# Optimization experiments

Hardware: AMD Instinct MI355X
Metric: run time of the kernel (lower is better)

## Reference

```python
import jax, jax.numpy as jnp
import numpy as np

DIM = 2048
N_HEADS = 32
N_KV_HEADS = 8
HEAD_DIM = DIM // N_HEADS  # 64
MAX_SEQ_LEN = 2048
ROPE_THETA = 10000.0
ROPE_SCALE = 1.0  # ("linear", 1.0)


def build_rope_cache(seq_len):
    # standard half-rotation RoPE cache with linear position scaling
    inv_freq = 1.0 / (ROPE_THETA ** (jnp.arange(0, HEAD_DIM, 2, dtype=jnp.float32) / HEAD_DIM))
    t = jnp.arange(seq_len, dtype=jnp.float32) / ROPE_SCALE
    freqs = jnp.outer(t, inv_freq)                      # [S, HD/2]
    emb = jnp.concatenate([freqs, freqs], axis=-1)      # [S, HD]
    return jnp.cos(emb), jnp.sin(emb)


def apply_rope(x, cos, sin):
    # x: [B, S, H, D]; cos/sin: [S, D]
    c = cos[None, :, None, :]
    s = sin[None, :, None, :]
    x1, x2 = jnp.split(x, 2, axis=-1)
    rot = jnp.concatenate([-x2, x1], axis=-1)           # rotate_half
    return x * c + rot * s


def setup_inputs() -> dict:
    key = jax.random.key(0)
    kx, kq, kk, kv, ko = jax.random.split(key, 5)
    B, S = 1, 2048
    x = jax.random.normal(kx, (B, S, DIM), dtype=jnp.float32)
    # nn.Linear weights stored [out_features, in_features]
    wq = jax.random.normal(kq, (DIM, DIM), dtype=jnp.float32) * 0.02
    wk = jax.random.normal(kk, (HEAD_DIM * N_KV_HEADS, DIM), dtype=jnp.float32) * 0.02
    wv = jax.random.normal(kv, (HEAD_DIM * N_KV_HEADS, DIM), dtype=jnp.float32) * 0.02
    wo = jax.random.normal(ko, (DIM, DIM), dtype=jnp.float32) * 0.02
    return {"x": x, "wq": wq, "wk": wk, "wv": wv, "wo": wo}


def reference(x, wq, wk, wv, wo):
    B, S, _ = x.shape
    g = N_HEADS // N_KV_HEADS  # GQA expand factor
    q = (x @ wq.T).reshape(B, S, N_HEADS, HEAD_DIM)
    k = (x @ wk.T).reshape(B, S, N_KV_HEADS, HEAD_DIM)
    v = (x @ wv.T).reshape(B, S, N_KV_HEADS, HEAD_DIM)
    cos, sin = build_rope_cache(S)
    q = apply_rope(q, cos, sin)
    k = apply_rope(k, cos, sin)
    # group q heads with their kv head instead of repeat_interleave on k/v
    q = q.transpose(0, 2, 1, 3).reshape(B, N_KV_HEADS, g, S, HEAD_DIM)
    k = k.transpose(0, 2, 1, 3)   # [B, Hkv, S, D]
    v = v.transpose(0, 2, 1, 3)
    scale = 1.0 / jnp.sqrt(jnp.asarray(HEAD_DIM, dtype=x.dtype))
    scores = jnp.einsum('bhgqd,bhkd->bhgqk', q, k) * scale  # [B,Hkv,g,S,S]
    causal = jnp.tril(jnp.ones((S, S), dtype=bool))
    scores = jnp.where(causal[None, None, None, :, :], scores, -jnp.inf)
    p = jax.nn.softmax(scores, axis=-1)
    out = jnp.einsum('bhgqk,bhkd->bhgqd', p, v)             # [B,Hkv,g,S,D]
    out = out.reshape(B, N_HEADS, S, HEAD_DIM).transpose(0, 2, 1, 3).reshape(B, S, DIM)
    return out @ wo.T
```

## Files before the change

kernel.cpp:

```cpp
#include <hip/hip_runtime.h>
#include <hip/hip_bf16.h>
#include <cstdint>
#include <cstddef>

#define DIM_ 2048
#define SLEN 2048
#define NQH 32
#define NKVH 8
#define HDIM 64
#define KVDIM 512

typedef __attribute__((ext_vector_type(8))) short short8;
typedef __attribute__((ext_vector_type(4))) float f32x4;
typedef __attribute__((ext_vector_type(16))) float f32x16;
typedef __attribute__((ext_vector_type(4))) unsigned int u32x4;

#define QSCALE 0.1803368801111243f

__device__ __forceinline__ unsigned short f2bf(float f) {
  unsigned u = __builtin_bit_cast(unsigned, f);
  u += 0x7FFFu + ((u >> 16) & 1u);
  return (unsigned short)(u >> 16);
}

__device__ __forceinline__ unsigned pack2bf(float a, float b) {
  return ((unsigned)f2bf(b) << 16) | (unsigned)f2bf(a);
}

__device__ __forceinline__ void gload_lds16(const void* g, void* l) {
  __builtin_amdgcn_global_load_lds(
      (const __attribute__((address_space(1))) void*)g,
      (__attribute__((address_space(3))) void*)l, 16, 0, 0);
}

__global__ void cvt_bf16_kernel(const float* __restrict__ in,
                                unsigned short* __restrict__ out, int n) {
  int i = (blockIdx.x * blockDim.x + threadIdx.x) * 8;
  if (i >= n) return;
  float4 a = *(const float4*)(in + i);
  float4 b = *(const float4*)(in + i + 4);
  ushort4 o0, o1;
  o0.x = f2bf(a.x); o0.y = f2bf(a.y); o0.z = f2bf(a.z); o0.w = f2bf(a.w);
  o1.x = f2bf(b.x); o1.y = f2bf(b.y); o1.z = f2bf(b.z); o1.w = f2bf(b.w);
  *(ushort4*)(out + i) = o0;
  *(ushort4*)(out + i + 4) = o1;
}

__global__ void rope_table_kernel(float* __restrict__ cosT, float* __restrict__ sinT) {
  int idx = blockIdx.x * blockDim.x + threadIdx.x;
  int s = idx >> 5, i = idx & 31;
  float inv = expf(-(float)i * (9.210340371976184f / 32.0f));
  float fr = (float)s * inv;
  cosT[idx] = cosf(fr);
  sinT[idx] = sinf(fr);
}

__global__ __launch_bounds__(256, 2)
void gemm_qkv(const unsigned short* __restrict__ A,
              const unsigned short* __restrict__ B,
              unsigned short* __restrict__ Qr,
              unsigned short* __restrict__ Kr,
              unsigned short* __restrict__ Vtp,
              const float* __restrict__ cosT,
              const float* __restrict__ sinT) {
  constexpr int K = DIM_;
  __shared__ unsigned short sA[128 * 32];
  __shared__ unsigned short sB[128 * 32];
  const int tid = threadIdx.x;
  const int wv = tid >> 6, ln = tid & 63;
  const int row0 = blockIdx.x * 128;
  const int col0 = blockIdx.y * 128;
  const int wr = (wv >> 1) * 64, wc = (wv & 1) * 64;
  const int lrow = ln & 15, lk = (ln >> 4) * 8;
  f32x4 acc[4][4] = {};

  for (int kt = 0; kt < K; kt += 32) {
#pragma unroll
    for (int r = 0; r < 2; ++r) {
      int e = (r * 256 + tid) * 8;
      int rr = e >> 5, cc = e & 31;
      gload_lds16(A + (size_t)(row0 + rr) * K + kt + cc,
                  sA + (size_t)(r * 256 + wv * 64) * 8);
      gload_lds16(B + (size_t)(col0 + rr) * K + kt + cc,
                  sB + (size_t)(r * 256 + wv * 64) * 8);
    }
    __syncthreads();
    short8 af[4], bfr[4];
#pragma unroll
    for (int m = 0; m < 4; ++m)
      af[m] = *(const short8*)(sA + (wr + m * 16 + lrow) * 32 + lk);
#pragma unroll
    for (int n = 0; n < 4; ++n)
      bfr[n] = *(const short8*)(sB + (wc + n * 16 + lrow) * 32 + lk);
#pragma unroll
    for (int m = 0; m < 4; ++m)
#pragma unroll
      for (int n = 0; n < 4; ++n)
        acc[m][n] = __builtin_amdgcn_mfma_f32_16x16x32_bf16(af[m], bfr[n],
                                                            acc[m][n], 0, 0, 0);
    __syncthreads();
  }
  const int orow = (ln >> 4) * 4;
  const int by = blockIdx.y;
  if (by < 16) {
#pragma unroll
    for (int m = 0; m < 4; ++m)
#pragma unroll
      for (int j = 0; j < 4; ++j) {
        const int s = row0 + wr + m * 16 + orow + j;
#pragma unroll
        for (int n = 0; n < 2; ++n) {
          const int d1 = n * 16 + lrow;
          const float cv = cosT[s * 32 + d1], sv = sinT[s * 32 + d1];
          const float x1 = acc[m][n][j], x2 = acc[m][n + 2][j];
          const size_t base = (size_t)s * DIM_ + col0 + wc + d1;
          Qr[base] = f2bf((x1 * cv - x2 * sv) * QSCALE);
          Qr[base + 32] = f2bf((x2 * cv + x1 * sv) * QSCALE);
        }
      }
  } else if (by < 20) {
    const int cb = col0 - 2048;
#pragma unroll
    for (int m = 0; m < 4; ++m)
#pragma unroll
      for (int j = 0; j < 4; ++j) {
        const int s = row0 + wr + m * 16 + orow + j;
#pragma unroll
        for (int n = 0; n < 2; ++n) {
          const int d1 = n * 16 + lrow;
          const float cv = cosT[s * 32 + d1], sv = sinT[s * 32 + d1];
          const float x1 = acc[m][n][j], x2 = acc[m][n + 2][j];
          const size_t base = (size_t)s * KVDIM + cb + wc + d1;
          Kr[base] = f2bf(x1 * cv - x2 * sv);
          Kr[base + 32] = f2bf(x2 * cv + x1 * sv);
        }
      }
  } else {
    const int cb = col0 - 2560;
#pragma unroll
    for (int m = 0; m < 4; ++m)
#pragma unroll
      for (int n = 0; n < 4; ++n)
#pragma unroll
        for (int j = 0; j < 4; ++j) {
          const int s = row0 + wr + m * 16 + orow + j;
          const int vc = cb + wc + n * 16 + lrow;
          Vtp[(size_t)vc * SLEN + s] = f2bf(acc[m][n][j]);
        }
  }
}

__global__ __launch_bounds__(256, 2)
void gemm_bt_f32(const unsigned short* __restrict__ A,
                 const unsigned short* __restrict__ B, float* __restrict__ C) {
  constexpr int K = DIM_;
  __shared__ unsigned short sA[128 * 32];
  __shared__ unsigned short sB[128 * 32];
  const int tid = threadIdx.x;
  const int wv = tid >> 6, ln = tid & 63;
  const int row0 = blockIdx.x * 128;
  const int col0 = blockIdx.y * 128;
  const int wr = (wv >> 1) * 64, wc = (wv & 1) * 64;
  const int lrow = ln & 15, lk = (ln >> 4) * 8;
  f32x4 acc[4][4] = {};
  for (int kt = 0; kt < K; kt += 32) {
#pragma unroll
    for (int r = 0; r < 2; ++r) {
      int e = (r * 256 + tid) * 8;
      int rr = e >> 5, cc = e & 31;
      gload_lds16(A + (size_t)(row0 + rr) * K + kt + cc,
                  sA + (size_t)(r * 256 + wv * 64) * 8);
      gload_lds16(B + (size_t)(col0 + rr) * K + kt + cc,
                  sB + (size_t)(r * 256 + wv * 64) * 8);
    }
    __syncthreads();
    short8 af[4], bfr[4];
#pragma unroll
    for (int m = 0; m < 4; ++m)
      af[m] = *(const short8*)(sA + (wr + m * 16 + lrow) * 32 + lk);
#pragma unroll
    for (int n = 0; n < 4; ++n)
      bfr[n] = *(const short8*)(sB + (wc + n * 16 + lrow) * 32 + lk);
#pragma unroll
    for (int m = 0; m < 4; ++m)
#pragma unroll
      for (int n = 0; n < 4; ++n)
        acc[m][n] = __builtin_amdgcn_mfma_f32_16x16x32_bf16(af[m], bfr[n],
                                                            acc[m][n], 0, 0, 0);
    __syncthreads();
  }
  const int orow = (ln >> 4) * 4;
#pragma unroll
  for (int m = 0; m < 4; ++m)
#pragma unroll
    for (int n = 0; n < 4; ++n)
#pragma unroll
      for (int j = 0; j < 4; ++j)
        C[(size_t)(row0 + wr + m * 16 + orow + j) * DIM_ + col0 + wc + n * 16 + lrow] =
            acc[m][n][j];
}

__global__ __launch_bounds__(256, 2)
void attn2_kernel(const unsigned short* __restrict__ Q,
                  const unsigned short* __restrict__ Kc,
                  const unsigned short* __restrict__ Vt,
                  unsigned short* __restrict__ AO) {
  __shared__ __align__(16) char smem[32768];
  const int b = blockIdx.x, h = blockIdx.y;
  const int kvh = h >> 2;
  const int tid = threadIdx.x;
  const int w = tid >> 6, l = tid & 63;
  const int l31 = l & 31, hi = l >> 5;
  const int kvcol = kvh * HDIM;

  int srow[2], scolb[2];
#pragma unroll
  for (int r = 0; r < 2; ++r) {
    int L = (r * 256 + tid) * 16;
    int row = L >> 7;
    srow[r] = row;
    scolb[r] = (L & 127) ^ ((row & 7) << 4);
  }

  for (int pass = 0; pass < 2; ++pass) {
    const int c = pass ? (15 - b) : b;
    const int nt = (c + 1) * 2;
    const int wq0 = c * 128 + w * 32;
    const int qrow = wq0 + l31;

    short8 qf[4];
    {
      const unsigned short* qp = Q + (size_t)qrow * DIM_ + h * HDIM + hi * 8;
#pragma unroll
      for (int dblk = 0; dblk < 4; ++dblk) qf[dblk] = *(const short8*)(qp + dblk * 16);
    }
    f32x16 o[2] = {};
    float mrun = -1e30f, lrun = 0.f;

#pragma unroll
    for (int r = 0; r < 2; ++r) {
      gload_lds16((const char*)Kc + (((size_t)srow[r] * KVDIM + kvcol) << 1) + scolb[r],
                  smem + r * 4096 + w * 1024);
      gload_lds16((const char*)Vt + (((size_t)(kvcol + srow[r]) * SLEN) << 1) + scolb[r],
                  smem + 16384 + r * 4096 + w * 1024);
    }
    __syncthreads();

    for (int t = 0; t < nt; ++t) {
      const int cur = t & 1;
      const int k0 = t * 64;
      if (t + 1 < nt) {
        const int nb = cur ^ 1;
        const int k0n = k0 + 64;
#pragma unroll
        for (int r = 0; r < 2; ++r) {
          gload_lds16((const char*)Kc + (((size_t)(k0n + srow[r]) * KVDIM + kvcol) << 1) + scolb[r],
                      smem + nb * 8192 + r * 4096 + w * 1024);
          gload_lds16((const char*)Vt + (((size_t)(kvcol + srow[r]) * SLEN + k0n) << 1) + scolb[r],
                      smem + 16384 + nb * 8192 + r * 4096 + w * 1024);
        }
      }
      if (k0 <= wq0 + 31) {
        const char* sK = smem + cur * 8192;
        const char* sV = smem + 16384 + cur * 8192;
        f32x16 s0 = {}, s1 = {};
        __builtin_amdgcn_s_setprio(1);
#pragma unroll
        for (int dblk = 0; dblk < 4; ++dblk) {
          const int colb = (dblk * 32 + hi * 16) ^ ((l31 & 7) << 4);
          short8 kf0 = *(const short8*)(sK + l31 * 128 + colb);
          short8 kf1 = *(const short8*)(sK + (32 + l31) * 128 + colb);
          s0 = __builtin_amdgcn_mfma_f32_32x32x16_bf16(kf0, qf[dblk], s0, 0, 0, 0);
          s1 = __builtin_amdgcn_mfma_f32_32x32x16_bf16(kf1, qf[dblk], s1, 0, 0, 0);
        }
        __builtin_amdgcn_s_setprio(0);

        float p[32];
#pragma unroll
        for (int r = 0; r < 16; ++r) { p[r] = s0[r]; p[16 + r] = s1[r]; }
        if (k0 + 63 > wq0) {
#pragma unroll
          for (int r = 0; r < 16; ++r) {
            const int ka = k0 + (r & 3) + 8 * (r >> 2) + 4 * hi;
            if (ka > qrow) p[r] = -1e30f;
            if (ka + 32 > qrow) p[16 + r] = -1e30f;
          }
        }
        float mt = p[0];
#pragma unroll
        for (int i = 1; i < 32; ++i) mt = fmaxf(mt, p[i]);
        mt = fmaxf(mt, __shfl_xor(mt, 32));
        const float mnew = fmaxf(mrun, mt);
        const float alpha = exp2f(mrun - mnew);
        mrun = mnew;
        float rs = 0.f;
#pragma unroll
        for (int i = 0; i < 32; ++i) { p[i] = exp2f(p[i] - mnew); rs += p[i]; }
        rs += __shfl_xor(rs, 32);
        lrun = lrun * alpha + rs;
#pragma unroll
        for (int r = 0; r < 16; ++r) { o[0][r] *= alpha; o[1][r] *= alpha; }

        unsigned pa[8], pb[8], sa[8], sb[8];
#pragma unroll
        for (int i = 0; i < 8; ++i) {
          pa[i] = pack2bf(p[i * 4 + 0], p[i * 4 + 1]);
          pb[i] = pack2bf(p[i * 4 + 2], p[i * 4 + 3]);
        }
#pragma unroll
        for (int i = 0; i < 8; ++i) {
          sa[i] = __shfl_xor((int)pa[i], 32);
          sb[i] = __shfl_xor((int)pb[i], 32);
        }
        __builtin_amdgcn_s_setprio(1);
#pragma unroll
        for (int kb = 0; kb < 4; ++kb) {
          const int i0 = (kb >> 1) * 4 + (kb & 1) * 2;
          const int i1 = i0 + 1;
          const unsigned w0 = hi ? sa[i1] : pa[i0];
          const unsigned w1 = hi ? sb[i1] : pb[i0];
          const unsigned w2 = hi ? pa[i1] : sa[i0];
          const unsigned w3 = hi ? pb[i1] : sb[i0];
          u32x4 uu = {w0, w1, w2, w3};
          short8 pf = __builtin_bit_cast(short8, uu);
          const int colb = (kb * 32 + hi * 16) ^ ((l31 & 7) << 4);
          short8 vf0 = *(const short8*)(sV + l31 * 128 + colb);
          short8 vf1 = *(const short8*)(sV + (32 + l31) * 128 + colb);
          o[0] = __builtin_amdgcn_mfma_f32_32x32x16_bf16(vf0, pf, o[0], 0, 0, 0);
          o[1] = __builtin_amdgcn_mfma_f32_32x32x16_bf16(vf1, pf, o[1], 0, 0, 0);
        }
        __builtin_amdgcn_s_setprio(0);
      }
      __syncthreads();
    }

    const float inv = 1.0f / lrun;
    char* tw = smem + w * 4096;
#pragma unroll
    for (int db = 0; db < 2; ++db)
#pragma unroll
      for (int g = 0; g < 4; ++g) {
        ushort4 v;
        v.x = f2bf(o[db][g * 4 + 0] * inv);
        v.y = f2bf(o[db][g * 4 + 1] * inv);
        v.z = f2bf(o[db][g * 4 + 2] * inv);
        v.w = f2bf(o[db][g * 4 + 3] * inv);
        const int d0 = db * 32 + g * 8 + hi * 4;
        *(ushort4*)(tw + l31 * 128 + ((d0 * 2) ^ ((l31 & 7) << 4))) = v;
      }
    {
      const int rr = l >> 1, cc = (l & 1) * 32;
      unsigned short* ap = AO + (size_t)(c * 128 + w * 32 + rr) * DIM_ + h * HDIM + cc;
#pragma unroll
      for (int pq = 0; pq < 4; ++pq) {
        const int colb = ((cc + pq * 8) * 2) ^ ((rr & 7) << 4);
        short8 v = *(const short8*)(tw + rr * 128 + colb);
        *(short8*)(ap + pq * 8) = v;
      }
    }
    __syncthreads();
  }
}

extern "C" void kernel_launch(void* const* d_in, const int* in_sizes, int n_in,
                              void* d_out, int out_size, void* d_ws, size_t ws_size,
                              hipStream_t stream) {
  const float* x  = (const float*)d_in[0];
  const float* wq = (const float*)d_in[1];
  const float* wk = (const float*)d_in[2];
  const float* wv = (const float*)d_in[3];
  const float* wo = (const float*)d_in[4];
  float* out = (float*)d_out;
  char* ws = (char*)d_ws;
  const size_t MB = 1u << 20;
  unsigned short* bx   = (unsigned short*)(ws + 0 * MB);
  unsigned short* bqkv = (unsigned short*)(ws + 8 * MB);
  unsigned short* bwo  = (unsigned short*)(ws + 20 * MB);
  unsigned short* Qr   = (unsigned short*)(ws + 28 * MB);
  unsigned short* Kr   = (unsigned short*)(ws + 36 * MB);
  unsigned short* Vt   = (unsigned short*)(ws + 38 * MB);
  unsigned short* AO   = (unsigned short*)(ws + 40 * MB);
  float* cosT = (float*)(ws + 48 * MB);
  float* sinT = (float*)(ws + 48 * MB + 256 * 1024);

  rope_table_kernel<<<SLEN * 32 / 256, 256, 0, stream>>>(cosT, sinT);
  cvt_bf16_kernel<<<(2048 * 2048 / 8) / 256, 256, 0, stream>>>(x, bx, 2048 * 2048);
  cvt_bf16_kernel<<<(2048 * 2048 / 8) / 256, 256, 0, stream>>>(wq, bqkv, 2048 * 2048);
  cvt_bf16_kernel<<<(512 * 2048 / 8) / 256, 256, 0, stream>>>(wk, bqkv + 2048 * 2048, 512 * 2048);
  cvt_bf16_kernel<<<(512 * 2048 / 8) / 256, 256, 0, stream>>>(wv, bqkv + 2560 * 2048, 512 * 2048);
  cvt_bf16_kernel<<<(2048 * 2048 / 8) / 256, 256, 0, stream>>>(wo, bwo, 2048 * 2048);

  gemm_qkv<<<dim3(16, 24), 256, 0, stream>>>(bx, bqkv, Qr, Kr, Vt, cosT, sinT);

  attn2_kernel<<<dim3(8, 32), 256, 0, stream>>>(Qr, Kr, Vt, AO);

  gemm_bt_f32<<<dim3(16, 16), 256, 0, stream>>>(AO, bwo, out);
}
```

Before: 253.3 us.

## Use 8-wave GEMM blocks, one-chunk-per-block attention with lazy rescale and permlane swaps

Both GEMMs move to 512-thread blocks with eight waves, each wave owning a 32x64 sub-tile, so each thread issues one LDS-direct load per operand per k-step. The attention kernel stops pairing two query chunks per block and launches 16x32 blocks, largest chunk first, with three blocks per CU allowed. The online softmax now skips the max/alpha rescale unless the new max exceeds the running one by more than 8 and uses tree reductions. P is packed with v_cvt_pk_bf16_f32 and exchanged across lane halves with v_permlane32_swap instead of shuffles. These target under-occupied GEMM blocks and shuffle and VALU overhead in attention, at the cost of less reuse per wave and more launched blocks.

```diff
diff --git a/kernel.cpp b/kernel.cpp
--- a/kernel.cpp
+++ b/kernel.cpp
@@ -23,8 +23,10 @@
   return (unsigned short)(u >> 16);
 }
 
-__device__ __forceinline__ unsigned pack2bf(float a, float b) {
-  return ((unsigned)f2bf(b) << 16) | (unsigned)f2bf(a);
+__device__ __forceinline__ unsigned cvt_pk_bf16(float lo, float hi) {
+  unsigned r;
+  asm("v_cvt_pk_bf16_f32 %0, %1, %2" : "=v"(r) : "v"(lo), "v"(hi));
+  return r;
 }
 
 __device__ __forceinline__ void gload_lds16(const void* g, void* l) {
@@ -55,7 +57,7 @@
   sinT[idx] = sinf(fr);
 }
 
-__global__ __launch_bounds__(256, 2)
+__global__ __launch_bounds__(512, 2)
 void gemm_qkv(const unsigned short* __restrict__ A,
               const unsigned short* __restrict__ B,
               unsigned short* __restrict__ Qr,
@@ -70,30 +72,24 @@
   const int wv = tid >> 6, ln = tid & 63;
   const int row0 = blockIdx.x * 128;
   const int col0 = blockIdx.y * 128;
-  const int wr = (wv >> 1) * 64, wc = (wv & 1) * 64;
+  const int wr = (wv >> 1) * 32, wc = (wv & 1) * 64;
   const int lrow = ln & 15, lk = (ln >> 4) * 8;
-  f32x4 acc[4][4] = {};
+  const int rr = tid >> 2, cc = (tid & 3) * 8;
+  f32x4 acc[2][4] = {};
 
   for (int kt = 0; kt < K; kt += 32) {
-#pragma unroll
-    for (int r = 0; r < 2; ++r) {
-      int e = (r * 256 + tid) * 8;
-      int rr = e >> 5, cc = e & 31;
-      gload_lds16(A + (size_t)(row0 + rr) * K + kt + cc,
-                  sA + (size_t)(r * 256 + wv * 64) * 8);
-      gload_lds16(B + (size_t)(col0 + rr) * K + kt + cc,
-                  sB + (size_t)(r * 256 + wv * 64) * 8);
-    }
-    __syncthreads();
-    short8 af[4], bfr[4];
-#pragma unroll
-    for (int m = 0; m < 4; ++m)
+    gload_lds16(A + (size_t)(row0 + rr) * K + kt + cc, sA + wv * 512);
+    gload_lds16(B + (size_t)(col0 + rr) * K + kt + cc, sB + wv * 512);
+    __syncthreads();
+    short8 af[2], bfr[4];
+#pragma unroll
+    for (int m = 0; m < 2; ++m)
       af[m] = *(const short8*)(sA + (wr + m * 16 + lrow) * 32 + lk);
 #pragma unroll
     for (int n = 0; n < 4; ++n)
       bfr[n] = *(const short8*)(sB + (wc + n * 16 + lrow) * 32 + lk);
 #pragma unroll
-    for (int m = 0; m < 4; ++m)
+    for (int m = 0; m < 2; ++m)
 #pragma unroll
       for (int n = 0; n < 4; ++n)
         acc[m][n] = __builtin_amdgcn_mfma_f32_16x16x32_bf16(af[m], bfr[n],
@@ -104,7 +100,7 @@
   const int by = blockIdx.y;
   if (by < 16) {
 #pragma unroll
-    for (int m = 0; m < 4; ++m)
+    for (int m = 0; m < 2; ++m)
 #pragma unroll
       for (int j = 0; j < 4; ++j) {
         const int s = row0 + wr + m * 16 + orow + j;
@@ -121,7 +117,7 @@
   } else if (by < 20) {
     const int cb = col0 - 2048;
 #pragma unroll
-    for (int m = 0; m < 4; ++m)
+    for (int m = 0; m < 2; ++m)
 #pragma unroll
       for (int j = 0; j < 4; ++j) {
         const int s = row0 + wr + m * 16 + orow + j;
@@ -138,7 +134,7 @@
   } else {
     const int cb = col0 - 2560;
 #pragma unroll
-    for (int m = 0; m < 4; ++m)
+    for (int m = 0; m < 2; ++m)
 #pragma unroll
       for (int n = 0; n < 4; ++n)
 #pragma unroll
@@ -150,7 +146,7 @@
   }
 }
 
-__global__ __launch_bounds__(256, 2)
+__global__ __launch_bounds__(512, 2)
 void gemm_bt_f32(const unsigned short* __restrict__ A,
                  const unsigned short* __restrict__ B, float* __restrict__ C) {
   constexpr int K = DIM_;
@@ -160,29 +156,23 @@
   const int wv = tid >> 6, ln = tid & 63;
   const int row0 = blockIdx.x * 128;
   const int col0 = blockIdx.y * 128;
-  const int wr = (wv >> 1) * 64, wc = (wv & 1) * 64;
+  const int wr = (wv >> 1) * 32, wc = (wv & 1) * 64;
   const int lrow = ln & 15, lk = (ln >> 4) * 8;
-  f32x4 acc[4][4] = {};
+  const int rr = tid >> 2, cc = (tid & 3) * 8;
+  f32x4 acc[2][4] = {};
   for (int kt = 0; kt < K; kt += 32) {
-#pragma unroll
-    for (int r = 0; r < 2; ++r) {
-      int e = (r * 256 + tid) * 8;
-      int rr = e >> 5, cc = e & 31;
-      gload_lds16(A + (size_t)(row0 + rr) * K + kt + cc,
-                  sA + (size_t)(r * 256 + wv * 64) * 8);
-      gload_lds16(B + (size_t)(col0 + rr) * K + kt + cc,
-                  sB + (size_t)(r * 256 + wv * 64) * 8);
-    }
-    __syncthreads();
-    short8 af[4], bfr[4];
-#pragma unroll
-    for (int m = 0; m < 4; ++m)
+    gload_lds16(A + (size_t)(row0 + rr) * K + kt + cc, sA + wv * 512);
+    gload_lds16(B + (size_t)(col0 + rr) * K + kt + cc, sB + wv * 512);
+    __syncthreads();
+    short8 af[2], bfr[4];
+#pragma unroll
+    for (int m = 0; m < 2; ++m)
       af[m] = *(const short8*)(sA + (wr + m * 16 + lrow) * 32 + lk);
 #pragma unroll
     for (int n = 0; n < 4; ++n)
       bfr[n] = *(const short8*)(sB + (wc + n * 16 + lrow) * 32 + lk);
 #pragma unroll
-    for (int m = 0; m < 4; ++m)
+    for (int m = 0; m < 2; ++m)
 #pragma unroll
       for (int n = 0; n < 4; ++n)
         acc[m][n] = __builtin_amdgcn_mfma_f32_16x16x32_bf16(af[m], bfr[n],
@@ -191,7 +181,7 @@
   }
   const int orow = (ln >> 4) * 4;
 #pragma unroll
-  for (int m = 0; m < 4; ++m)
+  for (int m = 0; m < 2; ++m)
 #pragma unroll
     for (int n = 0; n < 4; ++n)
 #pragma unroll
@@ -200,18 +190,21 @@
             acc[m][n][j];
 }
 
-__global__ __launch_bounds__(256, 2)
-void attn2_kernel(const unsigned short* __restrict__ Q,
+__global__ __launch_bounds__(256, 3)
+void attn3_kernel(const unsigned short* __restrict__ Q,
                   const unsigned short* __restrict__ Kc,
                   const unsigned short* __restrict__ Vt,
                   unsigned short* __restrict__ AO) {
   __shared__ __align__(16) char smem[32768];
-  const int b = blockIdx.x, h = blockIdx.y;
+  const int c = 15 - blockIdx.x, h = blockIdx.y;
   const int kvh = h >> 2;
   const int tid = threadIdx.x;
   const int w = tid >> 6, l = tid & 63;
   const int l31 = l & 31, hi = l >> 5;
   const int kvcol = kvh * HDIM;
+  const int nt = (c + 1) * 2;
+  const int wq0 = c * 128 + w * 32;
+  const int qrow = wq0 + l31;
 
   int srow[2], scolb[2];
 #pragma unroll
@@ -222,143 +215,145 @@
     scolb[r] = (L & 127) ^ ((row & 7) << 4);
   }
 
-  for (int pass = 0; pass < 2; ++pass) {
-    const int c = pass ? (15 - b) : b;
-    const int nt = (c + 1) * 2;
-    const int wq0 = c * 128 + w * 32;
-    const int qrow = wq0 + l31;
-
-    short8 qf[4];
-    {
-      const unsigned short* qp = Q + (size_t)qrow * DIM_ + h * HDIM + hi * 8;
-#pragma unroll
-      for (int dblk = 0; dblk < 4; ++dblk) qf[dblk] = *(const short8*)(qp + dblk * 16);
+  short8 qf[4];
+  {
+    const unsigned short* qp = Q + (size_t)qrow * DIM_ + h * HDIM + hi * 8;
+#pragma unroll
+    for (int dblk = 0; dblk < 4; ++dblk) qf[dblk] = *(const short8*)(qp + dblk * 16);
+  }
+  f32x16 o[2] = {};
+  float mrun = -1e30f, lrun = 0.f;
+
+#pragma unroll
+  for (int r = 0; r < 2; ++r) {
+    gload_lds16((const char*)Kc + (((size_t)srow[r] * KVDIM + kvcol) << 1) + scolb[r],
+                smem + r * 4096 + w * 1024);
+    gload_lds16((const char*)Vt + (((size_t)(kvcol + srow[r]) * SLEN) << 1) + scolb[r],
+                smem + 16384 + r * 4096 + w * 1024);
+  }
+  __syncthreads();
+
+  for (int t = 0; t < nt; ++t) {
+    const int cur = t & 1;
+    const int k0 = t * 64;
+    if (t + 1 < nt) {
+      const int nb = cur ^ 1;
+      const int k0n = k0 + 64;
+#pragma unroll
+      for (int r = 0; r < 2; ++r) {
+        gload_lds16((const char*)Kc + (((size_t)(k0n + srow[r]) * KVDIM + kvcol) << 1) + scolb[r],
+                    smem + nb * 8192 + r * 4096 + w * 1024);
+        gload_lds16((const char*)Vt + (((size_t)(kvcol + srow[r]) * SLEN + k0n) << 1) + scolb[r],
+                    smem + 16384 + nb * 8192 + r * 4096 + w * 1024);
+      }
     }
-    f32x16 o[2] = {};
-    float mrun = -1e30f, lrun = 0.f;
-
-#pragma unroll
-    for (int r = 0; r < 2; ++r) {
-      gload_lds16((const char*)Kc + (((size_t)srow[r] * KVDIM + kvcol) << 1) + scolb[r],
-                  smem + r * 4096 + w * 1024);
-      gload_lds16((const char*)Vt + (((size_t)(kvcol + srow[r]) * SLEN) << 1) + scolb[r],
-                  smem + 16384 + r * 4096 + w * 1024);
-    }
-    __syncthreads();
-
-    for (int t = 0; t < nt; ++t) {
-      const int cur = t & 1;
-      const int k0 = t * 64;
-      if (t + 1 < nt) {
-        const int nb = cur ^ 1;
-        const int k0n = k0 + 64;
-#pragma unroll
-        for (int r = 0; r < 2; ++r) {
-          gload_lds16((const char*)Kc + (((size_t)(k0n + srow[r]) * KVDIM + kvcol) << 1) + scolb[r],
-                      smem + nb * 8192 + r * 4096 + w * 1024);
-          gload_lds16((const char*)Vt + (((size_t)(kvcol + srow[r]) * SLEN + k0n) << 1) + scolb[r],
-                      smem + 16384 + nb * 8192 + r * 4096 + w * 1024);
+    if (k0 <= wq0 + 31) {
+      const char* sK = smem + cur * 8192;
+      const char* sV = smem + 16384 + cur * 8192;
+      f32x16 s0 = {}, s1 = {};
+      __builtin_amdgcn_s_setprio(1);
+#pragma unroll
+      for (int dblk = 0; dblk < 4; ++dblk) {
+        const int colb = (dblk * 32 + hi * 16) ^ ((l31 & 7) << 4);
+        short8 kf0 = *(const short8*)(sK + l31 * 128 + colb);
+        short8 kf1 = *(const short8*)(sK + (32 + l31) * 128 + colb);
+        s0 = __builtin_amdgcn_mfma_f32_32x32x16_bf16(kf0, qf[dblk], s0, 0, 0, 0);
+        s1 = __builtin_amdgcn_mfma_f32_32x32x16_bf16(kf1, qf[dblk], s1, 0, 0, 0);
+      }
+      __builtin_amdgcn_s_setprio(0);
+
+      float p[32];
+#pragma unroll
+      for (int r = 0; r < 16; ++r) { p[r] = s0[r]; p[16 + r] = s1[r]; }
+      if (k0 + 63 > wq0) {
+#pragma unroll
+        for (int r = 0; r < 16; ++r) {
+          const int ka = k0 + (r & 3) + 8 * (r >> 2) + 4 * hi;
+          if (ka > qrow) p[r] = -1e30f;
+          if (ka + 32 > qrow) p[16 + r] = -1e30f;
         }
       }
-      if (k0 <= wq0 + 31) {
-        const char* sK = smem + cur * 8192;
-        const char* sV = smem + 16384 + cur * 8192;
-        f32x16 s0 = {}, s1 = {};
-        __builtin_amdgcn_s_setprio(1);
-#pragma unroll
-        for (int dblk = 0; dblk < 4; ++dblk) {
-          const int colb = (dblk * 32 + hi * 16) ^ ((l31 & 7) << 4);
-          short8 kf0 = *(const short8*)(sK + l31 * 128 + colb);
-          short8 kf1 = *(const short8*)(sK + (32 + l31) * 128 + colb);
-          s0 = __builtin_amdgcn_mfma_f32_32x32x16_bf16(kf0, qf[dblk], s0, 0, 0, 0);
-          s1 = __builtin_amdgcn_mfma_f32_32x32x16_bf16(kf1, qf[dblk], s1, 0, 0, 0);
-        }
-        __builtin_amdgcn_s_setprio(0);
-
-        float p[32];
-#pragma unroll
-        for (int r = 0; r < 16; ++r) { p[r] = s0[r]; p[16 + r] = s1[r]; }
-        if (k0 + 63 > wq0) {
-#pragma unroll
-          for (int r = 0; r < 16; ++r) {
-            const int ka = k0 + (r & 3) + 8 * (r >> 2) + 4 * hi;
-            if (ka > qrow) p[r] = -1e30f;
-            if (ka + 32 > qrow) p[16 + r] = -1e30f;
-          }
-        }
-        float mt = p[0];
-#pragma unroll
-        for (int i = 1; i < 32; ++i) mt = fmaxf(mt, p[i]);
-        mt = fmaxf(mt, __shfl_xor(mt, 32));
-        const float mnew = fmaxf(mrun, mt);
+      float t16[16];
+#pragma unroll
+      for (int i = 0; i < 16; ++i) t16[i] = fmaxf(p[i], p[i + 16]);
+#pragma unroll
+      for (int i = 0; i < 8; ++i) t16[i] = fmaxf(t16[i], t16[i + 8]);
+#pragma unroll
+      for (int i = 0; i < 4; ++i) t16[i] = fmaxf(t16[i], t16[i + 4]);
+      float pmax = fmaxf(fmaxf(t16[0], t16[1]), fmaxf(t16[2], t16[3]));
+      pmax = fmaxf(pmax, __shfl_xor(pmax, 32));
+      if (!__all(pmax - mrun <= 8.0f)) {
+        const float mnew = fmaxf(mrun, pmax);
         const float alpha = exp2f(mrun - mnew);
         mrun = mnew;
-        float rs = 0.f;
-#pragma unroll
-        for (int i = 0; i < 32; ++i) { p[i] = exp2f(p[i] - mnew); rs += p[i]; }
-        rs += __shfl_xor(rs, 32);
-        lrun = lrun * alpha + rs;
+        lrun *= alpha;
 #pragma unroll
         for (int r = 0; r < 16; ++r) { o[0][r] *= alpha; o[1][r] *= alpha; }
-
-        unsigned pa[8], pb[8], sa[8], sb[8];
-#pragma unroll
-        for (int i = 0; i < 8; ++i) {
-          pa[i] = pack2bf(p[i * 4 + 0], p[i * 4 + 1]);
-          pb[i] = pack2bf(p[i * 4 + 2], p[i * 4 + 3]);
-        }
-#pragma unroll
-        for (int i = 0; i < 8; ++i) {
-          sa[i] = __shfl_xor((int)pa[i], 32);
-          sb[i] = __shfl_xor((int)pb[i], 32);
-        }
-        __builtin_amdgcn_s_setprio(1);
-#pragma unroll
-        for (int kb = 0; kb < 4; ++kb) {
-          const int i0 = (kb >> 1) * 4 + (kb & 1) * 2;
-          const int i1 = i0 + 1;
-          const unsigned w0 = hi ? sa[i1] : pa[i0];
-          const unsigned w1 = hi ? sb[i1] : pb[i0];
-          const unsigned w2 = hi ? pa[i1] : sa[i0];
-          const unsigned w3 = hi ? pb[i1] : sb[i0];
-          u32x4 uu = {w0, w1, w2, w3};
-          short8 pf = __builtin_bit_cast(short8, uu);
-          const int colb = (kb * 32 + hi * 16) ^ ((l31 & 7) << 4);
-          short8 vf0 = *(const short8*)(sV + l31 * 128 + colb);
-          short8 vf1 = *(const short8*)(sV + (32 + l31) * 128 + colb);
-          o[0] = __builtin_amdgcn_mfma_f32_32x32x16_bf16(vf0, pf, o[0], 0, 0, 0);
-          o[1] = __builtin_amdgcn_mfma_f32_32x32x16_bf16(vf1, pf, o[1], 0, 0, 0);
-        }
-        __builtin_amdgcn_s_setprio(0);
-      }
-      __syncthreads();
+      }
+#pragma unroll
+      for (int i = 0; i < 32; ++i) p[i] = exp2f(p[i] - mrun);
+      float u16[16];
+#pragma unroll
+      for (int i = 0; i < 16; ++i) u16[i] = p[i] + p[i + 16];
+#pragma unroll
+      for (int i = 0; i < 8; ++i) u16[i] += u16[i + 8];
+#pragma unroll
+      for (int i = 0; i < 4; ++i) u16[i] += u16[i + 4];
+      float rs = (u16[0] + u16[1]) + (u16[2] + u16[3]);
+      rs += __shfl_xor(rs, 32);
+      lrun += rs;
+
+      unsigned pa[8], pb[8];
+#pragma unroll
+      for (int i = 0; i < 8; ++i) {
+        pa[i] = cvt_pk_bf16(p[i * 4 + 0], p[i * 4 + 1]);
+        pb[i] = cvt_pk_bf16(p[i * 4 + 2], p[i * 4 + 3]);
+      }
+      __builtin_amdgcn_s_setprio(1);
+#pragma unroll
+      for (int kb = 0; kb < 4; ++kb) {
+        const int i0 = (kb >> 1) * 4 + (kb & 1) * 2;
+        const int i1 = i0 + 1;
+        unsigned w0 = pa[i0], w2 = pa[i1];
+        asm("v_permlane32_swap_b32 %0, %1" : "+v"(w0), "+v"(w2));
+        unsigned w1 = pb[i0], w3 = pb[i1];
+        asm("v_permlane32_swap_b32 %0, %1" : "+v"(w1), "+v"(w3));
+        u32x4 uu = {w0, w1, w2, w3};
+        short8 pf = __builtin_bit_cast(short8, uu);
+        const int colb = (kb * 32 + hi * 16) ^ ((l31 & 7) << 4);
+        short8 vf0 = *(const short8*)(sV + l31 * 128 + colb);
+        short8 vf1 = *(const short8*)(sV + (32 + l31) * 128 + colb);
+        o[0] = __builtin_amdgcn_mfma_f32_32x32x16_bf16(vf0, pf, o[0], 0, 0, 0);
+        o[1] = __builtin_amdgcn_mfma_f32_32x32x16_bf16(vf1, pf, o[1], 0, 0, 0);
+      }
+      __builtin_amdgcn_s_setprio(0);
     }
-
-    const float inv = 1.0f / lrun;
-    char* tw = smem + w * 4096;
-#pragma unroll
-    for (int db = 0; db < 2; ++db)
-#pragma unroll
-      for (int g = 0; g < 4; ++g) {
-        ushort4 v;
-        v.x = f2bf(o[db][g * 4 + 0] * inv);
-        v.y = f2bf(o[db][g * 4 + 1] * inv);
-        v.z = f2bf(o[db][g * 4 + 2] * inv);
-        v.w = f2bf(o[db][g * 4 + 3] * inv);
-        const int d0 = db * 32 + g * 8 + hi * 4;
-        *(ushort4*)(tw + l31 * 128 + ((d0 * 2) ^ ((l31 & 7) << 4))) = v;
-      }
-    {
-      const int rr = l >> 1, cc = (l & 1) * 32;
-      unsigned short* ap = AO + (size_t)(c * 128 + w * 32 + rr) * DIM_ + h * HDIM + cc;
-#pragma unroll
-      for (int pq = 0; pq < 4; ++pq) {
-        const int colb = ((cc + pq * 8) * 2) ^ ((rr & 7) << 4);
-        short8 v = *(const short8*)(tw + rr * 128 + colb);
-        *(short8*)(ap + pq * 8) = v;
-      }
+    __syncthreads();
+  }
+
+  const float inv = 1.0f / lrun;
+  char* tw = smem + w * 4096;
+#pragma unroll
+  for (int db = 0; db < 2; ++db)
+#pragma unroll
+    for (int g = 0; g < 4; ++g) {
+      ushort4 v;
+      v.x = f2bf(o[db][g * 4 + 0] * inv);
+      v.y = f2bf(o[db][g * 4 + 1] * inv);
+      v.z = f2bf(o[db][g * 4 + 2] * inv);
+      v.w = f2bf(o[db][g * 4 + 3] * inv);
+      const int d0 = db * 32 + g * 8 + hi * 4;
+      *(ushort4*)(tw + l31 * 128 + ((d0 * 2) ^ ((l31 & 7) << 4))) = v;
     }
-    __syncthreads();
+  {
+    const int rr = l >> 1, cc = (l & 1) * 32;
+    unsigned short* ap = AO + (size_t)(c * 128 + w * 32 + rr) * DIM_ + h * HDIM + cc;
+#pragma unroll
+    for (int pq = 0; pq < 4; ++pq) {
+      const int colb = ((cc + pq * 8) * 2) ^ ((rr & 7) << 4);
+      short8 v = *(const short8*)(tw + rr * 128 + colb);
+      *(short8*)(ap + pq * 8) = v;
+    }
   }
 }
 
@@ -390,9 +385,9 @@
   cvt_bf16_kernel<<<(512 * 2048 / 8) / 256, 256, 0, stream>>>(wv, bqkv + 2560 * 2048, 512 * 2048);
   cvt_bf16_kernel<<<(2048 * 2048 / 8) / 256, 256, 0, stream>>>(wo, bwo, 2048 * 2048);
 
-  gemm_qkv<<<dim3(16, 24), 256, 0, stream>>>(bx, bqkv, Qr, Kr, Vt, cosT, sinT);
-
-  attn2_kernel<<<dim3(8, 32), 256, 0, stream>>>(Qr, Kr, Vt, AO);
-
-  gemm_bt_f32<<<dim3(16, 16), 256, 0, stream>>>(AO, bwo, out);
-}
+  gemm_qkv<<<dim3(16, 24), 512, 0, stream>>>(bx, bqkv, Qr, Kr, Vt, cosT, sinT);
+
+  attn3_kernel<<<dim3(16, 32), 256, 0, stream>>>(Qr, Kr, Vt, AO);
+
+  gemm_bt_f32<<<dim3(16, 16), 512, 0, stream>>>(AO, bwo, out);
+}
```

New measurement: 257.5 us. Within noise of the previous version (+1.7%).
